# Performance work log

Measured on AMD Instinct MI355X. Metric: run time of the kernel, lower is better.

The kernel has to match this reference:

```python
import jax, jax.numpy as jnp
import numpy as np

N_NODES = 50000
N_EDGES = 800000
IN_DIM = 128
OUT_DIM = 128
NUM_EDGE_TYPES = 16
RULE_FEAT_DIM = 4


def setup_inputs() -> dict:
    key = jax.random.key(0)
    ks = jax.random.split(key, 20)
    d = OUT_DIM
    s_in = 1.0 / np.sqrt(IN_DIM)
    s_d = 1.0 / np.sqrt(d)
    s_r = 1.0 / np.sqrt(RULE_FEAT_DIM)
    inp = {
        "x": jax.random.normal(ks[0], (N_NODES, IN_DIM), jnp.float32),
        "edge_index": jax.random.randint(ks[1], (2, N_EDGES), 0, N_NODES),
        "edge_type": jax.random.randint(ks[2], (N_EDGES,), 0, NUM_EDGE_TYPES),
        "edge_rule_feat": jax.random.normal(ks[3], (N_EDGES, RULE_FEAT_DIM), jnp.float32),
        "total_nodes": N_NODES,
        # parameters (Linear stored as [in, out]; y = x @ W + b)
        "Wq": jax.random.uniform(ks[4], (IN_DIM, d), jnp.float32, -s_in, s_in),
        "bq": jnp.zeros((d,), jnp.float32),
        "Wk": jax.random.uniform(ks[5], (IN_DIM, d), jnp.float32, -s_in, s_in),
        "bk": jnp.zeros((d,), jnp.float32),
        "Wv": jax.random.uniform(ks[6], (IN_DIM, d), jnp.float32, -s_in, s_in),
        "bv": jnp.zeros((d,), jnp.float32),
        "rel_emb": jax.random.normal(ks[7], (NUM_EDGE_TYPES, d), jnp.float32),
        "attn_vec": jax.random.normal(ks[8], (3 * d,), jnp.float32),
        "rule_w1": jax.random.uniform(ks[9], (RULE_FEAT_DIM, d), jnp.float32, -s_r, s_r),
        "rule_b1": jnp.zeros((d,), jnp.float32),
        "rule_w2": jax.random.uniform(ks[10], (d, 1), jnp.float32, -s_d, s_d),
        "rule_b2": jnp.zeros((1,), jnp.float32),  # zero-initialized in source
        "gate_rule_w": jax.random.uniform(ks[11], (RULE_FEAT_DIM, 1), jnp.float32, -s_r, s_r),
        "gate_rule_b": jnp.zeros((1,), jnp.float32),
        "gate_neural_w": jax.random.uniform(ks[12], (2 * d, 1), jnp.float32, -1.0 / np.sqrt(2 * d), 1.0 / np.sqrt(2 * d)),
        "gate_neural_b": jnp.zeros((1,), jnp.float32),
        "msg_w": jax.random.uniform(ks[13], (d, d), jnp.float32, -s_d, s_d),
        "msg_b": jnp.zeros((d,), jnp.float32),
    }
    return inp


def reference(x, edge_index, edge_type, edge_rule_feat, total_nodes,
              Wq, bq, Wk, bk, Wv, bv, rel_emb, attn_vec,
              rule_w1, rule_b1, rule_w2, rule_b2,
              gate_rule_w, gate_rule_b, gate_neural_w, gate_neural_b,
              msg_w, msg_b):
    src, dst = edge_index[0], edge_index[1]
    d = msg_w.shape[0]

    h_src = x[src] @ Wk + bk                  # [E, d]
    h_dst = x[dst] @ Wq + bq                  # [E, d]
    rel = rel_emb[edge_type]                  # [E, d]

    # (cat([h_src,h_dst,rel]) * attn_vec).sum(-1) without materializing the concat
    a1, a2, a3 = attn_vec[:d], attn_vec[d:2 * d], attn_vec[2 * d:]
    e_base = jax.nn.leaky_relu(h_src @ a1 + h_dst @ a2 + rel @ a3, negative_slope=0.2)

    hidden = jax.nn.relu(edge_rule_feat @ rule_w1 + rule_b1)
    b_ij = (hidden @ rule_w2)[:, 0] + rule_b2[0]          # rule bias per edge

    gate_logit = (edge_rule_feat @ gate_rule_w)[:, 0] + gate_rule_b[0] \
               + (h_src @ gate_neural_w[:d, 0] + h_dst @ gate_neural_w[d:, 0]) + gate_neural_b[0]
    gamma_ij = jax.nn.sigmoid(gate_logit)

    e = e_base + gamma_ij * b_ij

    n = total_nodes
    # segment softmax over dst (numerically stable)
    seg_max = jax.ops.segment_max(e, dst, num_segments=n)
    e_exp = jnp.exp(e - seg_max[dst])
    seg_sum = jax.ops.segment_sum(e_exp, dst, num_segments=n)
    alpha = e_exp / (seg_sum[dst] + 1e-16)

    # eval mode: dropout is identity
    msg = ((x[src] @ Wv + bv + rel) @ msg_w + msg_b) * alpha[:, None]
    out = jax.ops.segment_sum(msg, dst, num_segments=n)   # index_add over dst
    return out, alpha, gamma_ij, b_ij
```

## Files before the change

### kernel.cpp

```cpp
#include <hip/hip_runtime.h>
#include <math.h>


using bf16x8 = __attribute__((ext_vector_type(8))) short;
using f32x4  = __attribute__((ext_vector_type(4))) float;

__device__ __forceinline__ float wave_max(float v) {
    #pragma unroll
    for (int o = 32; o > 0; o >>= 1) v = fmaxf(v, __shfl_xor(v, o, 64));
    return v;
}
__device__ __forceinline__ float wave_sum(float v) {
    #pragma unroll
    for (int o = 32; o > 0; o >>= 1) v += __shfl_xor(v, o, 64);
    return v;
}

__device__ __forceinline__ unsigned bf16rne(float f) {
    unsigned u = __float_as_uint(f);
    return (u + 0x7FFFu + ((u >> 16) & 1u)) >> 16;
}
__device__ __forceinline__ float bflo(unsigned u) { return __uint_as_float(u << 16); }
__device__ __forceinline__ float bfhi(unsigned u) { return __uint_as_float(u & 0xFFFF0000u); }

__global__ void __launch_bounds__(128) precompute_kernel(
    const float* __restrict__ Wq, const float* __restrict__ bq,
    const float* __restrict__ Wk, const float* __restrict__ bk,
    const float* __restrict__ Wv, const float* __restrict__ bv,
    const float* __restrict__ rel_emb, const float* __restrict__ attn_vec,
    const float* __restrict__ msg_w, const float* __restrict__ msg_b,
    const float* __restrict__ gnw, const float* __restrict__ grb,
    const float* __restrict__ gnb,
    const float* __restrict__ rule_w1, const float* __restrict__ rule_b1,
    const float* __restrict__ rule_w2,
    unsigned short* __restrict__ W2bT, float* __restrict__ c2,
    float* __restrict__ wkA, float* __restrict__ wqA,
    float* __restrict__ wkG, float* __restrict__ wqG,
    float* __restrict__ relA, float* __restrict__ relM,
    float* __restrict__ consts,
    float4* __restrict__ w1t, float2* __restrict__ w12)
{
    __shared__ float red[128];
    int bid = blockIdx.x, j = threadIdx.x;

    auto blk_reduce = [&](float v) -> float {
        red[j] = v;
        __syncthreads();
        for (int s = 64; s > 0; s >>= 1) {
            if (j < s) red[j] += red[j + s];
            __syncthreads();
        }
        float r = red[0];
        __syncthreads();
        return r;
    };

    if (bid < 128) {
        int i = bid;
        float acc = 0.f;
        #pragma unroll 8
        for (int k = 0; k < 128; ++k) acc = fmaf(Wv[i * 128 + k], msg_w[k * 128 + j], acc);
        W2bT[j * 128 + i] = (unsigned short)bf16rne(acc);
        float r;
        r = blk_reduce(Wk[i * 128 + j] * attn_vec[j]);        if (j == 0) wkA[i] = r;
        r = blk_reduce(Wq[i * 128 + j] * attn_vec[128 + j]);  if (j == 0) wqA[i] = r;
        r = blk_reduce(Wk[i * 128 + j] * gnw[j]);             if (j == 0) wkG[i] = r;
        r = blk_reduce(Wq[i * 128 + j] * gnw[128 + j]);       if (j == 0) wqG[i] = r;
    } else if (bid < 144) {
        int t = bid - 128;
        float acc = 0.f;
        #pragma unroll 8
        for (int k = 0; k < 128; ++k) acc = fmaf(rel_emb[t * 128 + k], msg_w[k * 128 + j], acc);
        relM[t * 128 + j] = acc;
        float r = blk_reduce(rel_emb[t * 128 + j] * attn_vec[256 + j]);
        if (j == 0) relA[t] = r;
    } else if (bid == 144) {
        float acc = msg_b[j];
        #pragma unroll 8
        for (int k = 0; k < 128; ++k) acc = fmaf(bv[k], msg_w[k * 128 + j], acc);
        c2[j] = acc;
        w1t[j] = make_float4(rule_w1[j], rule_w1[128 + j], rule_w1[256 + j], rule_w1[384 + j]);
        w12[j] = make_float2(rule_b1[j], rule_w2[j]);
    } else {
        float r = blk_reduce(bk[j] * attn_vec[j] + bq[j] * attn_vec[128 + j]);
        if (j == 0) consts[0] = r;
        r = blk_reduce(bk[j] * gnw[j] + bq[j] * gnw[128 + j]);
        if (j == 0) consts[1] = r + grb[0] + gnb[0];
    }
}

__global__ void __launch_bounds__(256) node_kernel(
    const float4* __restrict__ x4, const unsigned short* __restrict__ W2bT,
    const float* __restrict__ c2,
    const float* __restrict__ wkA, const float* __restrict__ wqA,
    const float* __restrict__ wkG, const float* __restrict__ wqG,
    unsigned* __restrict__ Vmb, float2* __restrict__ srcPack,
    float2* __restrict__ dstPack, int n_nodes)
{
    __shared__ unsigned short Asu[128][136];
    __shared__ unsigned short Bsu[128][136];
    const int tid = threadIdx.x;
    const int rowBase = blockIdx.x * 128;

    #pragma unroll
    for (int l = 0; l < 16; ++l) {
        int flat = l * 256 + tid;
        int r = flat >> 5, k4 = flat & 31;
        int row = rowBase + r;
        float4 v = (row < n_nodes) ? x4[row * 32 + k4] : make_float4(0.f, 0.f, 0.f, 0.f);
        uint2 u;
        u.x = bf16rne(v.x) | (bf16rne(v.y) << 16);
        u.y = bf16rne(v.z) | (bf16rne(v.w) << 16);
        *(uint2*)&Asu[r][k4 * 4] = u;
    }
    #pragma unroll
    for (int l = 0; l < 16; ++l) {
        int flat = l * 256 + tid;
        int n = flat >> 5, kq = flat & 31;
        uint2 w = *(const uint2*)&W2bT[n * 128 + kq * 4];
        *(uint2*)&Bsu[n][kq * 4] = w;
    }

    {
        int r = tid & 127, h = tid >> 7;
        int row = rowBase + r;
        if (row < n_nodes) {
            const float4* wa4 = (const float4*)(h ? wqA : wkA);
            const float4* wg4 = (const float4*)(h ? wqG : wkG);
            float sA = 0.f, sG = 0.f;
            #pragma unroll 8
            for (int k4 = 0; k4 < 32; ++k4) {
                float4 xv = x4[row * 32 + k4];
                float4 wa = wa4[k4], wg = wg4[k4];
                sA = fmaf(xv.x, wa.x, fmaf(xv.y, wa.y, fmaf(xv.z, wa.z, fmaf(xv.w, wa.w, sA))));
                sG = fmaf(xv.x, wg.x, fmaf(xv.y, wg.y, fmaf(xv.z, wg.z, fmaf(xv.w, wg.w, sG))));
            }
            if (h) dstPack[row] = make_float2(sA, sG);
            else   srcPack[row] = make_float2(sA, sG);
        }
    }
    __syncthreads();

    const int wave = tid >> 6, lane = tid & 63;
    const int ln = lane & 15, quad = lane >> 4;
    const int wm = (wave & 1) * 64, wn = (wave >> 1) * 64;

    f32x4 acc[4][4];
    #pragma unroll
    for (int i = 0; i < 4; ++i)
        #pragma unroll
        for (int j = 0; j < 4; ++j) acc[i][j] = (f32x4){0.f, 0.f, 0.f, 0.f};

    #pragma unroll
    for (int kc = 0; kc < 4; ++kc) {
        int k0 = kc * 32 + quad * 8;
        bf16x8 afr[4], bfr[4];
        #pragma unroll
        for (int mt = 0; mt < 4; ++mt)
            afr[mt] = *(const bf16x8*)&Asu[wm + mt * 16 + ln][k0];
        #pragma unroll
        for (int nt = 0; nt < 4; ++nt)
            bfr[nt] = *(const bf16x8*)&Bsu[wn + nt * 16 + ln][k0];
        #pragma unroll
        for (int mt = 0; mt < 4; ++mt)
            #pragma unroll
            for (int nt = 0; nt < 4; ++nt)
                acc[mt][nt] = __builtin_amdgcn_mfma_f32_16x16x32_bf16(
                    afr[mt], bfr[nt], acc[mt][nt], 0, 0, 0);
    }

    #pragma unroll
    for (int nt = 0; nt < 4; ++nt) {
        int col = wn + nt * 16 + ln;
        float cb = c2[col];
        #pragma unroll
        for (int mt = 0; mt < 4; ++mt) {
            #pragma unroll
            for (int r = 0; r < 4; ++r) {
                int row = rowBase + wm + mt * 16 + quad * 4 + r;
                float v = acc[mt][nt][r] + cb;
                float pv = __shfl_xor(v, 1, 64);
                if (!(ln & 1) && row < n_nodes) {
                    Vmb[row * 64 + (col >> 1)] = bf16rne(v) | (bf16rne(pv) << 16);
                }
            }
        }
    }
}

__global__ void __launch_bounds__(256) edge1a_kernel(
    const float4* __restrict__ erf, const int* __restrict__ dsts,
    const float4* __restrict__ w1t, const float2* __restrict__ w12,
    const float* __restrict__ rule_b2,
    float* __restrict__ b_out, int* __restrict__ hpart, int n_edges)
{
    __shared__ float4 s_w1t[128];
    __shared__ float2 s_w12[128];
    __shared__ int cnt[256];
    const int tid = threadIdx.x;
    if (tid < 128) { s_w1t[tid] = w1t[tid]; s_w12[tid] = w12[tid]; }
    cnt[tid] = 0;
    __syncthreads();

    const int eb = blockIdx.x * 2048;
    float4 rf[8];
    #pragma unroll
    for (int q = 0; q < 8; ++q) {
        int e = eb + q * 256 + tid;
        rf[q] = erf[min(e, n_edges - 1)];
        if (e < n_edges) atomicAdd(&cnt[dsts[e] >> 8], 1);
    }

    float bacc[8] = {0.f, 0.f, 0.f, 0.f, 0.f, 0.f, 0.f, 0.f};
    #pragma unroll 2
    for (int j = 0; j < 128; ++j) {
        float4 w = s_w1t[j];
        float2 c = s_w12[j];
        #pragma unroll
        for (int q = 0; q < 8; ++q) {
            float h = fmaf(rf[q].x, w.x, fmaf(rf[q].y, w.y,
                      fmaf(rf[q].z, w.z, fmaf(rf[q].w, w.w, c.x))));
            bacc[q] = fmaf(fmaxf(h, 0.f), c.y, bacc[q]);
        }
    }

    const float rb2 = rule_b2[0];
    #pragma unroll
    for (int q = 0; q < 8; ++q) {
        int e = eb + q * 256 + tid;
        if (e < n_edges) b_out[e] = bacc[q] + rb2;
    }
    __syncthreads();
    hpart[blockIdx.x * 256 + tid] = cnt[tid];
}

__global__ void __launch_bounds__(256) hred_kernel(
    const int* __restrict__ hpart, int* __restrict__ bucketTotal, int nblk)
{
    __shared__ int sdata[256];
    const int tid = threadIdx.x;
    const int b = blockIdx.x;
    int s = 0;
    for (int i = tid; i < nblk; i += 256) s += hpart[i * 256 + b];
    sdata[tid] = s;
    __syncthreads();
    #pragma unroll
    for (int off2 = 128; off2 > 0; off2 >>= 1) {
        if (tid < off2) sdata[tid] += sdata[tid + off2];
        __syncthreads();
    }
    if (tid == 0) bucketTotal[b] = sdata[0];
}

__global__ void __launch_bounds__(256) hscan_kernel(
    const int* __restrict__ bucketTotal, int* __restrict__ bucketCursor,
    int* __restrict__ bucketStart, int* __restrict__ rowPtr,
    int n_nodes, int n_edges)
{
    __shared__ int sdata[256];
    const int tid = threadIdx.x;
    int s = bucketTotal[tid];
    sdata[tid] = s;
    __syncthreads();
    #pragma unroll
    for (int off = 1; off < 256; off <<= 1) {
        int t = (tid >= off) ? sdata[tid - off] : 0;
        __syncthreads();
        sdata[tid] += t;
        __syncthreads();
    }
    int excl = sdata[tid] - s;
    bucketCursor[tid] = excl;
    bucketStart[tid] = excl;
    if (tid == 0) rowPtr[n_nodes] = n_edges;
}

__global__ void __launch_bounds__(256) sort1_kernel(
    const int* __restrict__ ei, const int* __restrict__ et,
    const float4* __restrict__ erf, const float* __restrict__ b_out,
    const float* __restrict__ grw,
    const float2* __restrict__ srcPack, const float2* __restrict__ dstPack,
    const float* __restrict__ relA, const float* __restrict__ consts,
    float* __restrict__ e_val, float* __restrict__ gamma_out,
    int* __restrict__ bucketCursor, float2* __restrict__ tmp, int n_edges)
{
    __shared__ float2 data[4096];
    __shared__ unsigned char slotB[4096];
    __shared__ int cnt[256], rk[256], base_[256], run[256], scanBuf[256];
    __shared__ float s_relA[16];
    const int tid = threadIdx.x;
    const int blockBase = blockIdx.x * 4096;
    const int total = min(4096, n_edges - blockBase);

    cnt[tid] = 0;
    rk[tid] = 0;
    if (tid < 16) s_relA[tid] = relA[tid];
    __syncthreads();

    const float c0 = consts[0], c1 = consts[1];
    const float g0 = grw[0], g1 = grw[1], g2 = grw[2], g3 = grw[3];

    int   d_[16];
    float ev_[16];
    int   pk_[16];
    #pragma unroll
    for (int i = 0; i < 16; ++i) {
        int e = blockBase + i * 256 + tid;
        if (e < n_edges) {
            int s = ei[e];
            int d = ei[n_edges + e];
            int t = et[e];
            float4 rf = erf[e];
            float b = b_out[e];
            float2 ss = srcPack[s], dd = dstPack[d];
            float pre = ss.x + dd.x + s_relA[t] + c0;
            float e_base = pre >= 0.f ? pre : 0.2f * pre;
            float gl = fmaf(rf.x, g0, fmaf(rf.y, g1,
                       fmaf(rf.z, g2, fmaf(rf.w, g3, c1 + ss.y + dd.y))));
            float gamma = 1.f / (1.f + __expf(-gl));
            float ev = e_base + gamma * b;
            gamma_out[e] = gamma;
            e_val[e] = ev;
            d_[i]  = d;
            ev_[i] = ev;
            pk_[i] = (s & 0xFFFF) | ((t & 15) << 16) | ((d & 255) << 20);
            atomicAdd(&cnt[d >> 8], 1);
        } else {
            d_[i] = -1;
        }
    }
    __syncthreads();

    int c = cnt[tid];
    scanBuf[tid] = c;
    __syncthreads();
    #pragma unroll
    for (int off = 1; off < 256; off <<= 1) {
        int t = (tid >= off) ? scanBuf[tid - off] : 0;
        __syncthreads();
        scanBuf[tid] += t;
        __syncthreads();
    }
    base_[tid] = scanBuf[tid] - c;
    run[tid] = c ? atomicAdd(&bucketCursor[tid], c) : 0;
    __syncthreads();

    #pragma unroll
    for (int i = 0; i < 16; ++i) {
        if (d_[i] >= 0) {
            int b = d_[i] >> 8;
            int r = atomicAdd(&rk[b], 1);
            int slot = base_[b] + r;
            data[slot] = make_float2(ev_[i], __int_as_float(pk_[i]));
            slotB[slot] = (unsigned char)b;
        }
    }
    __syncthreads();

    for (int j = tid; j < total; j += 256) {
        int b = slotB[j];
        tmp[run[b] + (j - base_[b])] = data[j];
    }
}

__global__ void __launch_bounds__(256) sort2_kernel(
    const int* __restrict__ bucketStart, const float2* __restrict__ tmp,
    float2* __restrict__ payload, int* __restrict__ rowPtr,
    int n_nodes, int n_edges, int nbuck)
{
    __shared__ int cnt[256], cur[256], sdata[256];
    const int tid = threadIdx.x;
    const int b = blockIdx.x;
    const int d0 = b * 256;
    const int lo = bucketStart[b];
    const int hi = (b == nbuck - 1) ? n_edges : bucketStart[b + 1];

    cnt[tid] = 0;
    __syncthreads();
    for (int j = lo + tid; j < hi; j += 256) {
        unsigned pk = __float_as_uint(tmp[j].y);
        atomicAdd(&cnt[(pk >> 20) & 255], 1);
    }
    __syncthreads();

    int c = cnt[tid];
    sdata[tid] = c;
    __syncthreads();
    #pragma unroll
    for (int off = 1; off < 256; off <<= 1) {
        int t = (tid >= off) ? sdata[tid - off] : 0;
        __syncthreads();
        sdata[tid] += t;
        __syncthreads();
    }
    int excl = sdata[tid] - c;
    cur[tid] = lo + excl;
    if (d0 + tid < n_nodes) rowPtr[d0 + tid] = lo + excl;
    __syncthreads();

    for (int j = lo + tid; j < hi; j += 256) {
        float2 p = tmp[j];
        unsigned pk = __float_as_uint(p.y);
        int dl = (pk >> 20) & 255;
        int pos = atomicAdd(&cur[dl], 1);
        unsigned st = (pk & 0xFFFFu) | (((pk >> 16) & 15u) << 27);
        payload[pos] = make_float2(p.x, __uint_as_float(st));
    }
}

__global__ void __launch_bounds__(256) gather_kernel(
    const int* __restrict__ rowPtr, const float2* __restrict__ payload,
    const unsigned* __restrict__ Vmb, const float* __restrict__ relM,
    float* __restrict__ out, float2* __restrict__ nodeMS, int n_nodes)
{
    __shared__ float2 s_relM[16 * 64];
    __shared__ float2 s_pay[4][64];
    __shared__ float  s_ts[4][16];
    const int tid = threadIdx.x;
    const float2* relM2 = (const float2*)relM;
    #pragma unroll
    for (int i = 0; i < 4; ++i) s_relM[i * 256 + tid] = relM2[i * 256 + tid];

    const int lane = tid & 63;
    const int w = tid >> 6;
    if (lane < 16) s_ts[w][lane] = 0.f;
    __syncthreads();

    int d = blockIdx.x * 4 + w;
    if (d >= n_nodes) return;
    int start = rowPtr[d];
    int deg = rowPtr[d + 1] - start;

    float acc0 = 0.f, acc1 = 0.f;
    float m = -INFINITY, inv;

    auto accrun = [&](int cnt) {
        for (int k = 0; k < cnt; k += 8) {
            float a[8];
            int ss[8];
            #pragma unroll
            for (int i = 0; i < 8; ++i) {
                float2 p = s_pay[w][k + i];
                a[i]  = p.x;
                ss[i] = __float_as_int(p.y) & 0x7FFFFFF;
            }
            unsigned v[8];
            #pragma unroll
            for (int i = 0; i < 8; ++i) v[i] = Vmb[ss[i] * 64 + lane];
            #pragma unroll
            for (int i = 0; i < 8; ++i) {
                acc0 = fmaf(a[i], bflo(v[i]), acc0);
                acc1 = fmaf(a[i], bfhi(v[i]), acc1);
            }
        }
    };

    if (deg <= 64) {
        float ev = -INFINITY;
        int st = 0;
        if (lane < deg) {
            float2 p = payload[start + lane];
            ev = p.x;
            st = __float_as_int(p.y);
        }
        m = wave_max(ev);
        float ex = (lane < deg) ? __expf(ev - m) : 0.f;
        float sum = wave_sum(ex);
        inv = 1.f / (sum + 1e-16f);
        float av = ex * inv;
        s_pay[w][lane] = make_float2(av, __int_as_float(st));
        if (lane < deg) atomicAdd(&s_ts[w][((unsigned)st) >> 27], av);
        accrun(deg);
    } else {
        for (int i = lane; i < deg; i += 64) m = fmaxf(m, payload[start + i].x);
        m = wave_max(m);
        float sum = 0.f;
        for (int i = lane; i < deg; i += 64) sum += __expf(payload[start + i].x - m);
        sum = wave_sum(sum);
        inv = 1.f / (sum + 1e-16f);
        for (int c = 0; c < deg; c += 64) {
            int i = c + lane;
            float av = 0.f;
            int st = 0;
            if (i < deg) {
                float2 p = payload[start + i];
                av = __expf(p.x - m) * inv;
                st = __float_as_int(p.y);
            }
            s_pay[w][lane] = make_float2(av, __int_as_float(st));
            if (i < deg) atomicAdd(&s_ts[w][((unsigned)st) >> 27], av);
            accrun(min(64, deg - c));
        }
    }

    #pragma unroll
    for (int t = 0; t < 16; ++t) {
        float ts = s_ts[w][t];
        float2 rm = s_relM[t * 64 + lane];
        acc0 = fmaf(ts, rm.x, acc0);
        acc1 = fmaf(ts, rm.y, acc1);
    }

    if (lane == 0) nodeMS[d] = make_float2(m, inv);
    *(float2*)&out[d * 128 + lane * 2] = make_float2(acc0, acc1);
}

__global__ void __launch_bounds__(256) alpha_kernel(
    const int* __restrict__ ei, const float* __restrict__ e_val,
    const float2* __restrict__ nodeMS, float* __restrict__ alpha_out, int n_edges)
{
    int e = blockIdx.x * blockDim.x + threadIdx.x;
    if (e >= n_edges) return;
    int d = ei[n_edges + e];
    float2 ms = nodeMS[d];
    alpha_out[e] = __expf(e_val[e] - ms.x) * ms.y;
}

extern "C" void kernel_launch(void* const* d_in, const int* in_sizes, int n_in,
                              void* d_out, int out_size, void* d_ws, size_t ws_size,
                              hipStream_t stream)
{
    const float* x        = (const float*)d_in[0];
    const int*   ei       = (const int*)d_in[1];
    const int*   et       = (const int*)d_in[2];
    const float* erf      = (const float*)d_in[3];
    const float* Wq       = (const float*)d_in[5];
    const float* bq       = (const float*)d_in[6];
    const float* Wk       = (const float*)d_in[7];
    const float* bk       = (const float*)d_in[8];
    const float* Wv       = (const float*)d_in[9];
    const float* bv       = (const float*)d_in[10];
    const float* rel_emb  = (const float*)d_in[11];
    const float* attn_vec = (const float*)d_in[12];
    const float* rule_w1  = (const float*)d_in[13];
    const float* rule_b1  = (const float*)d_in[14];
    const float* rule_w2  = (const float*)d_in[15];
    const float* rule_b2  = (const float*)d_in[16];
    const float* grw      = (const float*)d_in[17];
    const float* grb      = (const float*)d_in[18];
    const float* gnw      = (const float*)d_in[19];
    const float* gnb      = (const float*)d_in[20];
    const float* msg_w    = (const float*)d_in[21];
    const float* msg_b    = (const float*)d_in[22];

    const int n_nodes = in_sizes[0] / 128;
    const int n_edges = in_sizes[2];
    const int nab = (n_edges + 2047) / 2048;
    const int nhb = (n_edges + 4095) / 4096;
    const int nbuck = (n_nodes + 255) / 256;

    float* ws = (float*)d_ws;
    size_t off = 0;
    unsigned* Vmb  = (unsigned*)(ws + off); off += (size_t)n_nodes * 64;
    float2* payload = (float2*)(ws + off); off += 2 * (size_t)n_edges;
    float2* tmpPay  = (float2*)(ws + off); off += 2 * (size_t)n_edges;
    float* e_val   = ws + off; off += n_edges;
    float* srcPack = ws + off; off += 2 * (size_t)n_nodes;
    float* dstPack = ws + off; off += 2 * (size_t)n_nodes;
    float2* nodeMS = (float2*)(ws + off); off += 2 * (size_t)n_nodes;
    int*   rowPtr  = (int*)(ws + off); off += n_nodes + 4;
    int*   hpart   = (int*)(ws + off); off += (size_t)nab * 256;
    int*   bucketCursor = (int*)(ws + off); off += 256;
    int*   bucketStart  = (int*)(ws + off); off += 256;
    int*   bucketTotal  = (int*)(ws + off); off += 256;
    unsigned short* W2bT = (unsigned short*)(ws + off); off += 128 * 64;
    float* c2      = ws + off; off += 128;
    float* wkA     = ws + off; off += 128;
    float* wqA     = ws + off; off += 128;
    float* wkG     = ws + off; off += 128;
    float* wqG     = ws + off; off += 128;
    float* relA    = ws + off; off += 16;
    float* relM    = ws + off; off += 16 * 128;
    float* consts  = ws + off; off += 2;
    off += 2;
    float4* w1t    = (float4*)(ws + off); off += 128 * 4;
    float2* w12    = (float2*)(ws + off); off += 128 * 2;

    float* out       = (float*)d_out;
    float* alpha_out = out + (size_t)n_nodes * 128;
    float* gamma_out = alpha_out + n_edges;
    float* b_out     = gamma_out + n_edges;

    hipLaunchKernelGGL(precompute_kernel, dim3(146), dim3(128), 0, stream,
                       Wq, bq, Wk, bk, Wv, bv, rel_emb, attn_vec, msg_w, msg_b,
                       gnw, grb, gnb, rule_w1, rule_b1, rule_w2,
                       W2bT, c2, wkA, wqA, wkG, wqG, relA, relM, consts, w1t, w12);

    hipLaunchKernelGGL(node_kernel, dim3((n_nodes + 127) / 128), dim3(256), 0, stream,
                       (const float4*)x, W2bT, c2,
                       wkA, wqA, wkG, wqG, Vmb, (float2*)srcPack, (float2*)dstPack,
                       n_nodes);

    hipLaunchKernelGGL(edge1a_kernel, dim3(nab), dim3(256), 0, stream,
                       (const float4*)erf, ei + n_edges,
                       (const float4*)w1t, (const float2*)w12,
                       rule_b2, b_out, hpart, n_edges);

    hipLaunchKernelGGL(hred_kernel, dim3(256), dim3(256), 0, stream,
                       hpart, bucketTotal, nab);

    hipLaunchKernelGGL(hscan_kernel, dim3(1), dim3(256), 0, stream,
                       bucketTotal, bucketCursor, bucketStart, rowPtr,
                       n_nodes, n_edges);

    hipLaunchKernelGGL(sort1_kernel, dim3(nhb), dim3(256), 0, stream,
                       ei, et, (const float4*)erf, b_out, grw,
                       (const float2*)srcPack, (const float2*)dstPack,
                       relA, consts, e_val, gamma_out,
                       bucketCursor, tmpPay, n_edges);

    hipLaunchKernelGGL(sort2_kernel, dim3(nbuck), dim3(256), 0, stream,
                       bucketStart, tmpPay, payload, rowPtr,
                       n_nodes, n_edges, nbuck);

    hipLaunchKernelGGL(gather_kernel, dim3((n_nodes + 3) / 4), dim3(256), 0, stream,
                       rowPtr, payload, Vmb, relM, out, nodeMS, n_nodes);

    hipLaunchKernelGGL(alpha_kernel, dim3((n_edges + 255) / 256), dim3(256), 0, stream,
                       ei, e_val, nodeMS, alpha_out, n_edges);
}
```

Measured before the change: 271.0 us.

## Merge histogram reduce and scan, scatter sort1 directly, register-cache sort2

Replaces the two-kernel histogram reduction and scan with a single 1024-thread block that sums the per-block histograms and scans them, removing one launch. sort1 no longer stages edges in shared memory for a coalesced write. It scatters each edge directly to its global bucket slot, which removes the shared-memory buffers and the block scan but makes the global writes less coalesced. sort2 holds up to 24 strides of tmp in registers so the second pass does not reread global memory, at the cost of higher register pressure.

```diff
diff --git a/kernel.cpp b/kernel.cpp
--- a/kernel.cpp
+++ b/kernel.cpp
@@ -234,44 +234,35 @@
     hpart[blockIdx.x * 256 + tid] = cnt[tid];
 }
 
-__global__ void __launch_bounds__(256) hred_kernel(
-    const int* __restrict__ hpart, int* __restrict__ bucketTotal, int nblk)
-{
+__global__ void __launch_bounds__(1024) hscan2_kernel(
+    const int* __restrict__ hpart, int* __restrict__ bucketCursor,
+    int* __restrict__ bucketStart, int* __restrict__ rowPtr,
+    int nblk, int n_nodes, int n_edges)
+{
+    __shared__ int part[4][256];
     __shared__ int sdata[256];
     const int tid = threadIdx.x;
-    const int b = blockIdx.x;
+    const int b = tid & 255, g = tid >> 8;
     int s = 0;
-    for (int i = tid; i < nblk; i += 256) s += hpart[i * 256 + b];
-    sdata[tid] = s;
-    __syncthreads();
-    #pragma unroll
-    for (int off2 = 128; off2 > 0; off2 >>= 1) {
-        if (tid < off2) sdata[tid] += sdata[tid + off2];
+    for (int r = g; r < nblk; r += 4) s += hpart[r * 256 + b];
+    part[g][b] = s;
+    __syncthreads();
+    if (tid < 256) sdata[tid] = part[0][tid] + part[1][tid] + part[2][tid] + part[3][tid];
+    __syncthreads();
+    #pragma unroll
+    for (int off = 1; off < 256; off <<= 1) {
+        int t = 0;
+        if (tid < 256 && tid >= off) t = sdata[tid - off];
         __syncthreads();
-    }
-    if (tid == 0) bucketTotal[b] = sdata[0];
-}
-
-__global__ void __launch_bounds__(256) hscan_kernel(
-    const int* __restrict__ bucketTotal, int* __restrict__ bucketCursor,
-    int* __restrict__ bucketStart, int* __restrict__ rowPtr,
-    int n_nodes, int n_edges)
-{
-    __shared__ int sdata[256];
-    const int tid = threadIdx.x;
-    int s = bucketTotal[tid];
-    sdata[tid] = s;
-    __syncthreads();
-    #pragma unroll
-    for (int off = 1; off < 256; off <<= 1) {
-        int t = (tid >= off) ? sdata[tid - off] : 0;
+        if (tid < 256) sdata[tid] += t;
         __syncthreads();
-        sdata[tid] += t;
-        __syncthreads();
-    }
-    int excl = sdata[tid] - s;
-    bucketCursor[tid] = excl;
-    bucketStart[tid] = excl;
+    }
+    if (tid < 256) {
+        int tot = part[0][tid] + part[1][tid] + part[2][tid] + part[3][tid];
+        int excl = sdata[tid] - tot;
+        bucketCursor[tid] = excl;
+        bucketStart[tid] = excl;
+    }
     if (tid == 0) rowPtr[n_nodes] = n_edges;
 }
 
@@ -284,13 +275,10 @@
     float* __restrict__ e_val, float* __restrict__ gamma_out,
     int* __restrict__ bucketCursor, float2* __restrict__ tmp, int n_edges)
 {
-    __shared__ float2 data[4096];
-    __shared__ unsigned char slotB[4096];
-    __shared__ int cnt[256], rk[256], base_[256], run[256], scanBuf[256];
+    __shared__ int cnt[256], rk[256], run[256];
     __shared__ float s_relA[16];
     const int tid = threadIdx.x;
     const int blockBase = blockIdx.x * 4096;
-    const int total = min(4096, n_edges - blockBase);
 
     cnt[tid] = 0;
     rk[tid] = 0;
@@ -331,18 +319,7 @@
     }
     __syncthreads();
 
-    int c = cnt[tid];
-    scanBuf[tid] = c;
-    __syncthreads();
-    #pragma unroll
-    for (int off = 1; off < 256; off <<= 1) {
-        int t = (tid >= off) ? scanBuf[tid - off] : 0;
-        __syncthreads();
-        scanBuf[tid] += t;
-        __syncthreads();
-    }
-    base_[tid] = scanBuf[tid] - c;
-    run[tid] = c ? atomicAdd(&bucketCursor[tid], c) : 0;
+    if (cnt[tid]) run[tid] = atomicAdd(&bucketCursor[tid], cnt[tid]);
     __syncthreads();
 
     #pragma unroll
@@ -350,19 +327,12 @@
         if (d_[i] >= 0) {
             int b = d_[i] >> 8;
             int r = atomicAdd(&rk[b], 1);
-            int slot = base_[b] + r;
-            data[slot] = make_float2(ev_[i], __int_as_float(pk_[i]));
-            slotB[slot] = (unsigned char)b;
-        }
-    }
-    __syncthreads();
-
-    for (int j = tid; j < total; j += 256) {
-        int b = slotB[j];
-        tmp[run[b] + (j - base_[b])] = data[j];
-    }
-}
-
+            tmp[run[b] + r] = make_float2(ev_[i], __int_as_float(pk_[i]));
+        }
+    }
+}
+
+#define S2_MAXB 24
 __global__ void __launch_bounds__(256) sort2_kernel(
     const int* __restrict__ bucketStart, const float2* __restrict__ tmp,
     float2* __restrict__ payload, int* __restrict__ rowPtr,
@@ -377,10 +347,18 @@
 
     cnt[tid] = 0;
     __syncthreads();
-    for (int j = lo + tid; j < hi; j += 256) {
-        unsigned pk = __float_as_uint(tmp[j].y);
-        atomicAdd(&cnt[(pk >> 20) & 255], 1);
-    }
+
+    float2 v_[S2_MAXB];
+    #pragma unroll
+    for (int i = 0; i < S2_MAXB; ++i) {
+        int j = lo + i * 256 + tid;
+        if (j < hi) {
+            v_[i] = tmp[j];
+            atomicAdd(&cnt[(__float_as_uint(v_[i].y) >> 20) & 255], 1);
+        }
+    }
+    for (int j = lo + S2_MAXB * 256 + tid; j < hi; j += 256)
+        atomicAdd(&cnt[(__float_as_uint(tmp[j].y) >> 20) & 255], 1);
     __syncthreads();
 
     int c = cnt[tid];
@@ -398,7 +376,18 @@
     if (d0 + tid < n_nodes) rowPtr[d0 + tid] = lo + excl;
     __syncthreads();
 
-    for (int j = lo + tid; j < hi; j += 256) {
+    #pragma unroll
+    for (int i = 0; i < S2_MAXB; ++i) {
+        int j = lo + i * 256 + tid;
+        if (j < hi) {
+            unsigned pk = __float_as_uint(v_[i].y);
+            int dl = (pk >> 20) & 255;
+            int pos = atomicAdd(&cur[dl], 1);
+            unsigned st = (pk & 0xFFFFu) | (((pk >> 16) & 15u) << 27);
+            payload[pos] = make_float2(v_[i].x, __uint_as_float(st));
+        }
+    }
+    for (int j = lo + S2_MAXB * 256 + tid; j < hi; j += 256) {
         float2 p = tmp[j];
         unsigned pk = __float_as_uint(p.y);
         int dl = (pk >> 20) & 255;
@@ -562,7 +551,6 @@
     int*   hpart   = (int*)(ws + off); off += (size_t)nab * 256;
     int*   bucketCursor = (int*)(ws + off); off += 256;
     int*   bucketStart  = (int*)(ws + off); off += 256;
-    int*   bucketTotal  = (int*)(ws + off); off += 256;
     unsigned short* W2bT = (unsigned short*)(ws + off); off += 128 * 64;
     float* c2      = ws + off; off += 128;
     float* wkA     = ws + off; off += 128;
@@ -596,12 +584,9 @@
                        (const float4*)w1t, (const float2*)w12,
                        rule_b2, b_out, hpart, n_edges);
 
-    hipLaunchKernelGGL(hred_kernel, dim3(256), dim3(256), 0, stream,
-                       hpart, bucketTotal, nab);
-
-    hipLaunchKernelGGL(hscan_kernel, dim3(1), dim3(256), 0, stream,
-                       bucketTotal, bucketCursor, bucketStart, rowPtr,
-                       n_nodes, n_edges);
+    hipLaunchKernelGGL(hscan2_kernel, dim3(1), dim3(1024), 0, stream,
+                       hpart, bucketCursor, bucketStart, rowPtr,
+                       nab, n_nodes, n_edges);
 
     hipLaunchKernelGGL(sort1_kernel, dim3(nhb), dim3(256), 0, stream,
                        ei, et, (const float4*)erf, b_out, grw,
```

Result: slower. 281.8 us (+4.0%).
